# Kernel tuning notes

Measured on AMD Instinct MI355X. Metric: run time of the kernel, lower is better.

Reference implementation:

```python
import jax, jax.numpy as jnp
import numpy as np

B, L, d, D = 256, 128, 2, 128  # batch, sites, local dim, bond dim


def setup_inputs() -> dict:
    key = jax.random.key(0)
    k1, k2 = jax.random.split(key)
    # local quantum-number indices (output of hilbert.states_to_local_indices)
    x = jax.random.randint(k1, (B, L), 0, d, dtype=jnp.int32)
    # MPS unit-cell tensors: kernel_init (normal, std=0.01) + identity, as in setup()
    tensors = 0.01 * jax.random.normal(k2, (L, d, D, D), dtype=jnp.float32) \
        + jnp.eye(D, dtype=jnp.float32)
    return {"x": x, "tensors": tensors}


def reference(x, tensors):
    # x: (B, L) int indices in [0, d); tensors: (L, d, D, D)
    # symperiod == L so the tile in __call__ is a no-op.
    Bn, Ln = x.shape
    Dn = tensors.shape[-1]
    edge0 = jnp.broadcast_to(jnp.eye(Dn, dtype=tensors.dtype), (Bn, Dn, Dn))

    @jax.checkpoint
    def step(edge, pair):
        site_tensors, qn = pair          # (d, D, D), (B,)
        a = site_tensors[qn]             # gather per-sample matrix -> (B, D, D)
        return edge @ a, None            # batched (B,D,D)@(B,D,D)

    edge, _ = jax.lax.scan(step, edge0, (tensors, x.T))
    psi = jnp.trace(edge, axis1=-2, axis2=-1)     # (B,)
    return jnp.log(psi.astype(jnp.complex64))
```

## Files before the change

kernel.cpp:

```cpp
#include <hip/hip_runtime.h>
#include <cstdint>

#define DD   128
#define LL   128
#define MAT  (DD*DD)
#define ROWB 256

typedef float  f32x16 __attribute__((ext_vector_type(16)));
typedef short  bf16x8 __attribute__((ext_vector_type(8)));
typedef unsigned short u16_t;

__device__ u16_t g_A  [LL*2*MAT];
__device__ u16_t g_At [LL*2*MAT];
__device__ u16_t g_M2 [64*4*MAT];
__device__ u16_t g_M2t[64*4*MAT];
__device__ u16_t g_M4t[32*16*MAT];
__device__ u16_t g_F0 [256*MAT];
__device__ u16_t g_F1 [256*MAT];

__device__ __forceinline__ u16_t f2bf(float f){
  unsigned int x = __builtin_bit_cast(unsigned int, f);
  unsigned int r = (x + 0x7FFFu + ((x >> 16) & 1u)) >> 16;
  return (u16_t)r;
}
__device__ __forceinline__ float bf2f(u16_t u){
  unsigned int x = ((unsigned int)u) << 16;
  return __builtin_bit_cast(float, x);
}
__device__ __forceinline__ f32x16 mfma32(bf16x8 a, bf16x8 b, f32x16 c){
  return __builtin_amdgcn_mfma_f32_32x32x16_bf16(a, b, c, 0, 0, 0);
}
__device__ __forceinline__ f32x16 zero16(){
  f32x16 z;
#pragma unroll
  for (int i = 0; i < 16; ++i) z[i] = 0.f;
  return z;
}
__device__ __forceinline__ unsigned cvtpk(float lo, float hi){
  unsigned r;
  asm("v_cvt_pk_bf16_f32 %0, %1, %2" : "=v"(r) : "v"(lo), "v"(hi));
  return r;
}
__device__ __forceinline__ void pl32swap(unsigned &a, unsigned &b){
  asm volatile("v_permlane32_swap_b32 %0, %1" : "+v"(a), "+v"(b));
}

__device__ __forceinline__ void stage32k(char* dstLds, const u16_t* srcG, int ltid){
  int w4 = ltid >> 6, l = ltid & 63;
  const char* g = (const char*)srcG + w4*8192 + l*16;
  char* s = dstLds + w4*8192;
#pragma unroll
  for (int i = 0; i < 8; ++i){
    __builtin_amdgcn_global_load_lds(
      (const __attribute__((address_space(1))) unsigned int*)(uintptr_t)(g + i*1024),
      (__attribute__((address_space(3))) unsigned int*)(unsigned int)(uintptr_t)(s + i*1024),
      16, 0, 0);
  }
}

__global__ __launch_bounds__(256, 1) void k_convert(const float* __restrict__ T){
  __shared__ float tile[128][129];
  const int lq = blockIdx.x, tid = threadIdx.x;
  const float* src = T + (size_t)lq * MAT;
#pragma unroll 4
  for (int i = 0; i < 64; ++i){
    int idx = tid + 256*i;
    float v = src[idx];
    g_A[lq*MAT + idx] = f2bf(v);
    tile[idx >> 7][idx & 127] = v;
  }
  __syncthreads();
#pragma unroll 4
  for (int i = 0; i < 64; ++i){
    int idx = tid + 256*i;
    int c = idx >> 7, k = idx & 127;
    g_At[lq*MAT + idx] = f2bf(tile[k][c]);
  }
}

__global__ __launch_bounds__(256, 1) void k_prod(int level){
  __shared__ u16_t CT[MAT];
  __shared__ u16_t CR[MAT];
  const int bid = blockIdx.x, tid = threadIdx.x;
  const int w = tid >> 6, lane = tid & 63, g = lane >> 5, ln = lane & 31;
  const int wr = (w >> 1) * 64, wc = (w & 1) * 64;

  const u16_t *X, *Yt; u16_t *Z, *Zt;
  if (level == 1){
    int p = bid >> 2, c2 = bid & 3;
    X  = g_A  + ((2*p)*2   + (c2 & 1)) * MAT;
    Yt = g_At + ((2*p+1)*2 + ((c2 >> 1) & 1)) * MAT;
    Z  = g_M2  + bid*MAT;
    Zt = g_M2t + bid*MAT;
  } else {
    int gg = bid >> 4, c = bid & 15;
    X  = g_M2  + ((2*gg)*4   + (c & 3)) * MAT;
    Yt = g_M2t + ((2*gg+1)*4 + (c >> 2)) * MAT;
    Z  = nullptr;
    Zt = g_M4t + bid*MAT;
  }

  f32x16 acc[2][2];
  acc[0][0] = zero16(); acc[0][1] = zero16();
  acc[1][0] = zero16(); acc[1][1] = zero16();

#pragma unroll
  for (int kw = 0; kw < 8; ++kw){
    int ko = kw*32 + g*16;
    bf16x8 a0 = *(const bf16x8*)((const char*)X  + (wr + ln     )*ROWB + ko);
    bf16x8 a1 = *(const bf16x8*)((const char*)X  + (wr + 32 + ln)*ROWB + ko);
    bf16x8 b0 = *(const bf16x8*)((const char*)Yt + (wc + ln     )*ROWB + ko);
    bf16x8 b1 = *(const bf16x8*)((const char*)Yt + (wc + 32 + ln)*ROWB + ko);
    acc[0][0] = mfma32(a0, b0, acc[0][0]);
    acc[0][1] = mfma32(a0, b1, acc[0][1]);
    acc[1][0] = mfma32(a1, b0, acc[1][0]);
    acc[1][1] = mfma32(a1, b1, acc[1][1]);
  }

#pragma unroll
  for (int mt = 0; mt < 2; ++mt){
#pragma unroll
    for (int nt = 0; nt < 2; ++nt){
      int c  = wc + nt*32 + ln;
      int xc = (c & 15) << 4;
#pragma unroll
      for (int q = 0; q < 4; ++q){
        int r4 = wr + mt*32 + 8*q + 4*g;
        unsigned int lo = (unsigned)f2bf(acc[mt][nt][4*q+0]) | ((unsigned)f2bf(acc[mt][nt][4*q+1]) << 16);
        unsigned int hi = (unsigned)f2bf(acc[mt][nt][4*q+2]) | ((unsigned)f2bf(acc[mt][nt][4*q+3]) << 16);
        uint2 v; v.x = lo; v.y = hi;
        *(uint2*)((char*)CT + c*ROWB + ((2*r4) ^ xc)) = v;
      }
      if (level == 1){
#pragma unroll
        for (int i = 0; i < 16; ++i){
          int r = wr + mt*32 + (i & 3) + 8*(i >> 2) + 4*g;
          *(u16_t*)((char*)CR + r*ROWB + ((2*c) ^ ((r & 15) << 4))) = f2bf(acc[mt][nt][i]);
        }
      }
    }
  }
  __syncthreads();

  if (level == 1){
#pragma unroll
    for (int i = 0; i < 8; ++i){
      int o = (tid + 256*i) * 16;
      int row = o >> 8, wb = o & 255;
      int xr = (row & 15) << 4;
      uint4 vt = *(const uint4*)((const char*)CT + row*ROWB + (wb ^ xr));
      *(uint4*)((char*)Zt + o) = vt;
      uint4 vz = *(const uint4*)((const char*)CR + row*ROWB + (wb ^ xr));
      *(uint4*)((char*)Z + o) = vz;
    }
  } else {
#pragma unroll
    for (int i = 0; i < 8; ++i){
      int o = tid + 256*i;
      int lnn = o & 31, ggg = (o >> 5) & 1, kww = (o >> 6) & 7, rtt = o >> 9;
      int r = 32*rtt + lnn;
      int srcB = r*ROWB + ((32*kww + 16*ggg) ^ ((r & 15) << 4));
      uint4 vt = *(const uint4*)((const char*)CT + srcB);
      *(uint4*)((char*)Zt + o*16) = vt;
    }
  }
}

#define LDS_MAIN (2*32768 + 64)

__global__ __launch_bounds__(256, 1) void k_main(const int* __restrict__ x){
  extern __shared__ char lds[];
  char* bufs  = lds;
  int*  combo = (int*)(lds + 2*32768);

  const int bid = blockIdx.x;
  const int b = bid & 255, half = bid >> 8;
  const int tid = threadIdx.x;
  const int w = tid >> 6, lane = tid & 63, g = lane >> 5, ln = lane & 31;

  if (tid < 16){
    const int* xb = x + b*LL + (half*16 + tid)*4;
    combo[tid] = (xb[0] & 1) | ((xb[1] & 1) << 1) | ((xb[2] & 1) << 2) | ((xb[3] & 1) << 3);
  }

  uint4 F[8];
#pragma unroll
  for (int kw = 0; kw < 8; ++kw){
    unsigned wd[4] = {0u,0u,0u,0u};
#pragma unroll
    for (int j = 0; j < 8; ++j){
      int k = 16*kw + 8*g + j;
      if (k == 32*w + ln) wd[j >> 1] |= 0x3F80u << (16*(j & 1));
    }
    uint4 v; v.x = wd[0]; v.y = wd[1]; v.z = wd[2]; v.w = wd[3];
    F[kw] = v;
  }
  __syncthreads();

  stage32k(bufs, g_M4t + (size_t)((half*16)*16 + combo[0])*MAT, tid);

  for (int s = 0; s < 16; ++s){
    const char* Mc = bufs + (s & 1)*32768;
    char*       Mn = bufs + ((s + 1) & 1)*32768;
    if (s + 1 < 16){
      stage32k(Mn, g_M4t + (size_t)((half*16 + s + 1)*16 + combo[s+1])*MAT, tid);
      asm volatile("s_waitcnt vmcnt(8)" ::: "memory");
    } else {
      asm volatile("s_waitcnt vmcnt(0)" ::: "memory");
    }
    __builtin_amdgcn_s_barrier();
    __builtin_amdgcn_sched_barrier(0);

    const char* Ml = Mc + lane*16;

    f32x16 acc[4];
#pragma unroll
    for (int rt = 0; rt < 4; ++rt) acc[rt] = zero16();

#pragma unroll
    for (int kw = 0; kw < 8; ++kw){
      bf16x8 bb = __builtin_bit_cast(bf16x8, F[kw]);
#pragma unroll
      for (int rt = 0; rt < 4; ++rt){
        bf16x8 a = *(const bf16x8*)(Ml + (rt*8 + kw)*1024);
        acc[rt] = mfma32(a, bb, acc[rt]);
      }
    }

#pragma unroll
    for (int rt = 0; rt < 4; ++rt){
      unsigned y0 = cvtpk(acc[rt][0],  acc[rt][1]);
      unsigned x0 = cvtpk(acc[rt][4],  acc[rt][5]);
      pl32swap(y0, x0);
      unsigned y1 = cvtpk(acc[rt][2],  acc[rt][3]);
      unsigned x1 = cvtpk(acc[rt][6],  acc[rt][7]);
      pl32swap(y1, x1);
      uint4 v0; v0.x = y0; v0.y = y1; v0.z = x0; v0.w = x1;
      F[2*rt] = v0;

      unsigned y2 = cvtpk(acc[rt][8],  acc[rt][9]);
      unsigned x2 = cvtpk(acc[rt][12], acc[rt][13]);
      pl32swap(y2, x2);
      unsigned y3 = cvtpk(acc[rt][10], acc[rt][11]);
      unsigned x3 = cvtpk(acc[rt][14], acc[rt][15]);
      pl32swap(y3, x3);
      uint4 v1; v1.x = y2; v1.y = y3; v1.z = x2; v1.w = x3;
      F[2*rt+1] = v1;
    }
    __builtin_amdgcn_sched_barrier(0);
    __builtin_amdgcn_s_barrier();
  }

  const int c = 32*w + ln;
  if (half == 0){
    u16_t* dst = g_F0 + (size_t)b*MAT + c*128;
#pragma unroll
    for (int kw = 0; kw < 8; ++kw)
      *(uint4*)(dst + kw*16 + g*8) = F[kw];
  } else {
    u16_t* dst = g_F1 + (size_t)b*MAT + c;
#pragma unroll
    for (int kw = 0; kw < 8; ++kw){
      uint4 v = F[kw];
      unsigned wd[4] = {v.x, v.y, v.z, v.w};
#pragma unroll
      for (int j = 0; j < 8; ++j){
        int k = 16*kw + 8*g + j;
        u16_t bits = (u16_t)((j & 1) ? (wd[j >> 1] >> 16) : (wd[j >> 1] & 0xFFFF));
        dst[(size_t)k*128] = bits;
      }
    }
  }
}

__global__ __launch_bounds__(256, 1) void k_tail(float* __restrict__ out,
                                                 int out_complex){
  __shared__ float red[4];
  const int b = blockIdx.x, tid = threadIdx.x;
  const int w = tid >> 6, lane = tid & 63;

  const u16_t* S0 = g_F0 + (size_t)b*MAT;
  const u16_t* W  = g_F1 + (size_t)b*MAT;

  float sum = 0.f;
#pragma unroll
  for (int i = 0; i < 8; ++i){
    int o = (i*256 + tid)*8;
    uint4 a = *(const uint4*)(S0 + o);
    uint4 v = *(const uint4*)(W  + o);
    unsigned aw[4] = {a.x, a.y, a.z, a.w};
    unsigned vw[4] = {v.x, v.y, v.z, v.w};
#pragma unroll
    for (int q = 0; q < 4; ++q){
      sum += bf2f((u16_t)(aw[q] & 0xFFFF)) * bf2f((u16_t)(vw[q] & 0xFFFF));
      sum += bf2f((u16_t)(aw[q] >> 16))    * bf2f((u16_t)(vw[q] >> 16));
    }
  }
#pragma unroll
  for (int off = 1; off < 64; off <<= 1) sum += __shfl_xor(sum, off, 64);
  if (lane == 0) red[w] = sum;
  __syncthreads();
  if (tid == 0){
    float s = red[0] + red[1] + red[2] + red[3];
    float re = logf(fabsf(s));
    float im = (s < 0.f) ? 3.14159265358979323f : 0.f;
    if (out_complex){ out[2*b] = re; out[2*b+1] = im; }
    else            { out[b] = re; }
  }
}

extern "C" void kernel_launch(void* const* d_in, const int* in_sizes, int n_in,
                              void* d_out, int out_size, void* d_ws, size_t ws_size,
                              hipStream_t stream){
  const int*   x = (const int*)d_in[0];
  const float* T = (const float*)d_in[1];
  int Bn = in_sizes[0] / LL;
  int oc = (out_size >= 2*Bn) ? 1 : 0;

  (void)d_ws; (void)ws_size; (void)n_in;
  hipFuncSetAttribute(reinterpret_cast<const void*>(k_main),
                      hipFuncAttributeMaxDynamicSharedMemorySize, LDS_MAIN);

  k_convert<<<LL*2,  256, 0, stream>>>(T);
  k_prod   <<<256,   256, 0, stream>>>(1);
  k_prod   <<<512,   256, 0, stream>>>(2);
  k_main   <<<2*Bn,  256, LDS_MAIN, stream>>>(x);
  k_tail   <<<Bn,    256, 0, stream>>>((float*)d_out, oc);
}
```

Before: 77.15 us.

## Merge both chain halves into one block, two waves per chain

k_main now runs one block per batch sample instead of two. Each block holds both half-chains (waves 0-1 and waves 2-3), each with its own double-buffered 64KB LDS region. Each wave now computes 64 columns as two 32-column fragments, so every A-operand load from LDS feeds two MFMAs. The x bits are gathered with a wave ballot rather than an LDS combo table. This halves grid size and raises register and LDS use per block, trading parallelism across CUs for more reuse of each staged tile.

```diff
diff --git a/kernel.cpp b/kernel.cpp
--- a/kernel.cpp
+++ b/kernel.cpp
@@ -51,6 +51,19 @@
   char* s = dstLds + w4*8192;
 #pragma unroll
   for (int i = 0; i < 8; ++i){
+    __builtin_amdgcn_global_load_lds(
+      (const __attribute__((address_space(1))) unsigned int*)(uintptr_t)(g + i*1024),
+      (__attribute__((address_space(3))) unsigned int*)(unsigned int)(uintptr_t)(s + i*1024),
+      16, 0, 0);
+  }
+}
+
+__device__ __forceinline__ void stage32k128(char* dstLds, const u16_t* srcG, int ltid){
+  int w2 = ltid >> 6, l = ltid & 63;
+  const char* g = (const char*)srcG + w2*16384 + l*16;
+  char* s = dstLds + w2*16384;
+#pragma unroll
+  for (int i = 0; i < 16; ++i){
     __builtin_amdgcn_global_load_lds(
       (const __attribute__((address_space(1))) unsigned int*)(uintptr_t)(g + i*1024),
       (__attribute__((address_space(3))) unsigned int*)(unsigned int)(uintptr_t)(s + i*1024),
@@ -166,45 +179,48 @@
   }
 }
 
-#define LDS_MAIN (2*32768 + 64)
+#define LDS_MAIN (4*32768)
 
 __global__ __launch_bounds__(256, 1) void k_main(const int* __restrict__ x){
   extern __shared__ char lds[];
-  char* bufs  = lds;
-  int*  combo = (int*)(lds + 2*32768);
-
-  const int bid = blockIdx.x;
-  const int b = bid & 255, half = bid >> 8;
-  const int tid = threadIdx.x;
-  const int w = tid >> 6, lane = tid & 63, g = lane >> 5, ln = lane & 31;
-
-  if (tid < 16){
-    const int* xb = x + b*LL + (half*16 + tid)*4;
-    combo[tid] = (xb[0] & 1) | ((xb[1] & 1) << 1) | ((xb[2] & 1) << 2) | ((xb[3] & 1) << 3);
-  }
-
-  uint4 F[8];
-#pragma unroll
-  for (int kw = 0; kw < 8; ++kw){
-    unsigned wd[4] = {0u,0u,0u,0u};
-#pragma unroll
-    for (int j = 0; j < 8; ++j){
-      int k = 16*kw + 8*g + j;
-      if (k == 32*w + ln) wd[j >> 1] |= 0x3F80u << (16*(j & 1));
-    }
-    uint4 v; v.x = wd[0]; v.y = wd[1]; v.z = wd[2]; v.w = wd[3];
-    F[kw] = v;
-  }
-  __syncthreads();
-
-  stage32k(bufs, g_M4t + (size_t)((half*16)*16 + combo[0])*MAT, tid);
+
+  const int b = blockIdx.x, tid = threadIdx.x;
+  const int w8 = tid >> 6, lane = tid & 63, g = lane >> 5, ln = lane & 31;
+  const int chain = w8 >> 1, wpos = w8 & 1, ltid = tid & 127;
+  char* chainBuf = lds + chain*65536;
+
+  int xv = x[b*LL + chain*64 + lane] & 1;
+  unsigned long long bits = __ballot(xv != 0);
+
+  uint4 F[2][8];
+#pragma unroll
+  for (int f = 0; f < 2; ++f){
+    int c = 64*wpos + 32*f + ln;
+#pragma unroll
+    for (int kw = 0; kw < 8; ++kw){
+      unsigned wd[4] = {0u,0u,0u,0u};
+#pragma unroll
+      for (int j = 0; j < 8; ++j){
+        int k = 16*kw + 8*g + j;
+        if (k == c) wd[j >> 1] |= 0x3F80u << (16*(j & 1));
+      }
+      uint4 v; v.x = wd[0]; v.y = wd[1]; v.z = wd[2]; v.w = wd[3];
+      F[f][kw] = v;
+    }
+  }
+
+  {
+    int cb0 = (int)(bits & 15ull);
+    stage32k128(chainBuf, g_M4t + (size_t)((chain*16)*16 + cb0)*MAT, ltid);
+  }
 
   for (int s = 0; s < 16; ++s){
-    const char* Mc = bufs + (s & 1)*32768;
-    char*       Mn = bufs + ((s + 1) & 1)*32768;
+    const char* Mc = chainBuf + (s & 1)*32768;
+    char*       Mn = chainBuf + ((s + 1) & 1)*32768;
     if (s + 1 < 16){
-      stage32k(Mn, g_M4t + (size_t)((half*16 + s + 1)*16 + combo[s+1])*MAT, tid);
-      asm volatile("s_waitcnt vmcnt(8)" ::: "memory");
+      int cb = (int)((bits >> (4*(s+1))) & 15ull);
+      stage32k128(Mn, g_M4t + (size_t)((chain*16 + s + 1)*16 + cb)*MAT, ltid);
+      asm volatile("s_waitcnt vmcnt(16)" ::: "memory");
     } else {
       asm volatile("s_waitcnt vmcnt(0)" ::: "memory");
     }
@@ -213,61 +229,75 @@
 
     const char* Ml = Mc + lane*16;
 
-    f32x16 acc[4];
-#pragma unroll
-    for (int rt = 0; rt < 4; ++rt) acc[rt] = zero16();
+    f32x16 acc[2][4];
+#pragma unroll
+    for (int f = 0; f < 2; ++f)
+#pragma unroll
+      for (int rt = 0; rt < 4; ++rt) acc[f][rt] = zero16();
 
 #pragma unroll
     for (int kw = 0; kw < 8; ++kw){
-      bf16x8 bb = __builtin_bit_cast(bf16x8, F[kw]);
+      bf16x8 b0 = __builtin_bit_cast(bf16x8, F[0][kw]);
+      bf16x8 b1 = __builtin_bit_cast(bf16x8, F[1][kw]);
 #pragma unroll
       for (int rt = 0; rt < 4; ++rt){
         bf16x8 a = *(const bf16x8*)(Ml + (rt*8 + kw)*1024);
-        acc[rt] = mfma32(a, bb, acc[rt]);
-      }
-    }
-
-#pragma unroll
-    for (int rt = 0; rt < 4; ++rt){
-      unsigned y0 = cvtpk(acc[rt][0],  acc[rt][1]);
-      unsigned x0 = cvtpk(acc[rt][4],  acc[rt][5]);
-      pl32swap(y0, x0);
-      unsigned y1 = cvtpk(acc[rt][2],  acc[rt][3]);
-      unsigned x1 = cvtpk(acc[rt][6],  acc[rt][7]);
-      pl32swap(y1, x1);
-      uint4 v0; v0.x = y0; v0.y = y1; v0.z = x0; v0.w = x1;
-      F[2*rt] = v0;
-
-      unsigned y2 = cvtpk(acc[rt][8],  acc[rt][9]);
-      unsigned x2 = cvtpk(acc[rt][12], acc[rt][13]);
-      pl32swap(y2, x2);
-      unsigned y3 = cvtpk(acc[rt][10], acc[rt][11]);
-      unsigned x3 = cvtpk(acc[rt][14], acc[rt][15]);
-      pl32swap(y3, x3);
-      uint4 v1; v1.x = y2; v1.y = y3; v1.z = x2; v1.w = x3;
-      F[2*rt+1] = v1;
+        acc[0][rt] = mfma32(a, b0, acc[0][rt]);
+        acc[1][rt] = mfma32(a, b1, acc[1][rt]);
+      }
+    }
+
+#pragma unroll
+    for (int f = 0; f < 2; ++f){
+#pragma unroll
+      for (int rt = 0; rt < 4; ++rt){
+        unsigned y0 = cvtpk(acc[f][rt][0],  acc[f][rt][1]);
+        unsigned x0 = cvtpk(acc[f][rt][4],  acc[f][rt][5]);
+        pl32swap(y0, x0);
+        unsigned y1 = cvtpk(acc[f][rt][2],  acc[f][rt][3]);
+        unsigned x1 = cvtpk(acc[f][rt][6],  acc[f][rt][7]);
+        pl32swap(y1, x1);
+        uint4 v0; v0.x = y0; v0.y = y1; v0.z = x0; v0.w = x1;
+        F[f][2*rt] = v0;
+
+        unsigned y2 = cvtpk(acc[f][rt][8],  acc[f][rt][9]);
+        unsigned x2 = cvtpk(acc[f][rt][12], acc[f][rt][13]);
+        pl32swap(y2, x2);
+        unsigned y3 = cvtpk(acc[f][rt][10], acc[f][rt][11]);
+        unsigned x3 = cvtpk(acc[f][rt][14], acc[f][rt][15]);
+        pl32swap(y3, x3);
+        uint4 v1; v1.x = y2; v1.y = y3; v1.z = x2; v1.w = x3;
+        F[f][2*rt+1] = v1;
+      }
     }
     __builtin_amdgcn_sched_barrier(0);
     __builtin_amdgcn_s_barrier();
   }
 
-  const int c = 32*w + ln;
-  if (half == 0){
-    u16_t* dst = g_F0 + (size_t)b*MAT + c*128;
-#pragma unroll
-    for (int kw = 0; kw < 8; ++kw)
-      *(uint4*)(dst + kw*16 + g*8) = F[kw];
+  if (chain == 0){
+#pragma unroll
+    for (int f = 0; f < 2; ++f){
+      int c = 64*wpos + 32*f + ln;
+      u16_t* dst = g_F0 + (size_t)b*MAT + c*128;
+#pragma unroll
+      for (int kw = 0; kw < 8; ++kw)
+        *(uint4*)(dst + kw*16 + g*8) = F[f][kw];
+    }
   } else {
-    u16_t* dst = g_F1 + (size_t)b*MAT + c;
-#pragma unroll
-    for (int kw = 0; kw < 8; ++kw){
-      uint4 v = F[kw];
-      unsigned wd[4] = {v.x, v.y, v.z, v.w};
-#pragma unroll
-      for (int j = 0; j < 8; ++j){
-        int k = 16*kw + 8*g + j;
-        u16_t bits = (u16_t)((j & 1) ? (wd[j >> 1] >> 16) : (wd[j >> 1] & 0xFFFF));
-        dst[(size_t)k*128] = bits;
+#pragma unroll
+    for (int f = 0; f < 2; ++f){
+      int c = 64*wpos + 32*f + ln;
+      u16_t* dst = g_F1 + (size_t)b*MAT + c;
+#pragma unroll
+      for (int kw = 0; kw < 8; ++kw){
+        uint4 v = F[f][kw];
+        unsigned wd[4] = {v.x, v.y, v.z, v.w};
+#pragma unroll
+        for (int j = 0; j < 8; ++j){
+          int k = 16*kw + 8*g + j;
+          u16_t bb = (u16_t)((j & 1) ? (wd[j >> 1] >> 16) : (wd[j >> 1] & 0xFFFF));
+          dst[(size_t)k*128] = bb;
+        }
       }
     }
   }
@@ -321,9 +351,9 @@
   hipFuncSetAttribute(reinterpret_cast<const void*>(k_main),
                       hipFuncAttributeMaxDynamicSharedMemorySize, LDS_MAIN);
 
-  k_convert<<<LL*2,  256, 0, stream>>>(T);
-  k_prod   <<<256,   256, 0, stream>>>(1);
-  k_prod   <<<512,   256, 0, stream>>>(2);
-  k_main   <<<2*Bn,  256, LDS_MAIN, stream>>>(x);
-  k_tail   <<<Bn,    256, 0, stream>>>((float*)d_out, oc);
-}
+  k_convert<<<LL*2, 256, 0, stream>>>(T);
+  k_prod   <<<256,  256, 0, stream>>>(1);
+  k_prod   <<<512,  256, 0, stream>>>(2);
+  k_main   <<<Bn,   256, LDS_MAIN, stream>>>(x);
+  k_tail   <<<Bn,   256, 0, stream>>>((float*)d_out, oc);
+}
```

Measured after the change: 82.51 us. +6.9%, slower.
